# Performance work log

Measured on AMD Instinct MI355X. Metric: run time of the kernel, lower is better.

The kernel has to match this reference:

```python
import math
import jax, jax.numpy as jnp
import numpy as np

B, N, CS, CZ, CH, H, PQ, PV = 1, 4096, 512, 128, 64, 16, 4, 8
BQ, BK = 32, 128
NB = N // BQ
CZ4 = CZ // 4
INF = 100000.0
EPS = 1e-8


def quat_to_rot(q):
    w, x, y, z = q[..., 0], q[..., 1], q[..., 2], q[..., 3]
    return jnp.stack([
        jnp.stack([1 - 2 * (y * y + z * z), 2 * (x * y - w * z), 2 * (x * z + w * y)], -1),
        jnp.stack([2 * (x * y + w * z), 1 - 2 * (x * x + z * z), 2 * (y * z - w * x)], -1),
        jnp.stack([2 * (x * z - w * y), 2 * (y * z + w * x), 1 - 2 * (x * x + y * y)], -1),
    ], -2)


def setup_inputs() -> dict:
    key = jax.random.key(0)
    ks = jax.random.split(key, 16)
    s = jax.random.normal(ks[0], (B, N, CS), jnp.float32)
    z = jax.random.normal(ks[1], (B, NB, BQ, BK, CZ), jnp.float32)
    trans = jax.random.normal(ks[2], (B, N, 3), jnp.float32) * 10.0
    quat = jax.random.normal(ks[3], (B, N, 4), jnp.float32)
    quat = quat / jnp.linalg.norm(quat, axis=-1, keepdims=True)
    rots = quat_to_rot(quat)
    s_mask = jnp.ones((B, N), jnp.float32)
    pad = (BK - BQ) // 2  # key window centered on each query block
    key_idx = (jnp.arange(NB)[:, None] * BQ - pad + jnp.arange(BK)[None, :]).astype(jnp.int32)

    def w(k, shp):
        return jax.random.normal(k, shp, jnp.float32) * (1.0 / math.sqrt(shp[0]))

    return {
        's': s, 'z': z, 'trans': trans, 'rots': rots, 's_mask': s_mask, 'key_idx': key_idx,
        'Wq': w(ks[4], (CS, H * CH)), 'Wk': w(ks[5], (CS, H * CH)), 'Wv': w(ks[6], (CS, H * CH)),
        'Wqp': w(ks[7], (CS, H * PQ * 3)), 'Wkvp': w(ks[8], (CS, H * (PQ + PV) * 3)),
        'Wb': w(ks[9], (CZ, H)), 'Wdz': w(ks[10], (CZ, CZ4)),
        'head_weights': jnp.full((H,), float(np.log(np.e - 1.0)), jnp.float32),  # softplus^-1(1)
        'Wout': w(ks[11], (H * (CZ4 + CH + PV * 4), CS)),
        'g_s': jnp.ones((CS,), jnp.float32), 'b_s': jnp.zeros((CS,), jnp.float32),
        'g_z': jnp.ones((CZ,), jnp.float32), 'b_z': jnp.zeros((CZ,), jnp.float32),
    }


def _ln(x, g, b):
    m = jnp.mean(x, -1, keepdims=True)
    v = jnp.mean((x - m) ** 2, -1, keepdims=True)
    return (x - m) * jax.lax.rsqrt(v + 1e-5) * g + b


def _ipa(s, z, trans, rots, s_mask, key_idx, Wq, Wk, Wv, Wqp, Wkvp, Wb, Wdz,
         head_weights, Wout, g_s, b_s, g_z, b_z):
    s_n = _ln(s, g_s, b_s)
    z_n = _ln(z, g_z, b_z)

    valid = (key_idx >= 0) & (key_idx < N)            # [NB, BK]
    idx = jnp.clip(key_idx, 0, N - 1)
    vf = valid.astype(s.dtype)[None]                  # [1, NB, BK]

    def gk(x):  # gather key window: [B,N,...] -> [B,NB,BK,...]
        return x[:, idx]

    sq = s_n.reshape(B, NB, BQ, CS)
    sk = gk(s_n) * vf[..., None]                      # zero-pad out-of-range keys

    tq = trans.reshape(B, NB, BQ, 3)
    rq = rots.reshape(B, NB, BQ, 3, 3)
    tk = gk(trans) * vf[..., None]
    rk = jnp.where(valid[None, :, :, None, None], gk(rots), jnp.eye(3, dtype=rots.dtype))

    q = (sq @ Wq).reshape(B, NB, BQ, H, CH)
    k = (sk @ Wk).reshape(B, NB, BK, H, CH)
    v = (sk @ Wv).reshape(B, NB, BK, H, CH)

    q_pts = (sq @ Wqp).reshape(B, NB, BQ, H * PQ, 3)
    q_pts = jnp.einsum('bnqij,bnqpj->bnqpi', rq, q_pts) + tq[:, :, :, None, :]
    q_pts = q_pts.reshape(B, NB, BQ, H, PQ, 3)

    kv_pts = (sk @ Wkvp).reshape(B, NB, BK, H * (PQ + PV), 3)
    kv_pts = jnp.einsum('bnkij,bnkpj->bnkpi', rk, kv_pts) + tk[:, :, :, None, :]
    kv_pts = kv_pts.reshape(B, NB, BK, H, PQ + PV, 3)
    k_pts, v_pts = kv_pts[..., :PQ, :], kv_pts[..., PQ:, :]

    bias = jnp.einsum('bnqkc,ch->bnqkh', z_n, Wb)
    a = jnp.einsum('bnqhc,bnkhc->bnqkh', q, k) * math.sqrt(1.0 / (3 * CH))
    a = a + math.sqrt(1.0 / 3) * bias

    disp = q_pts[:, :, :, None] - k_pts[:, :, None]   # [B,NB,BQ,BK,H,PQ,3]
    pt_att = jnp.sum(disp ** 2, -1)                   # [B,NB,BQ,BK,H,PQ]
    hw = jax.nn.softplus(head_weights) * math.sqrt(1.0 / (3 * (PQ * 9.0 / 2)))
    pt_att = -0.5 * jnp.sum(pt_att * hw[:, None], -1)  # [B,NB,BQ,BK,H]

    qm = s_mask.reshape(B, NB, BQ)
    km = gk(s_mask) * vf
    amask = INF * (qm[:, :, :, None] * km[:, :, None, :] - 1.0)

    a = a + pt_att + amask[..., None]
    a = jax.nn.softmax(jnp.swapaxes(a, -1, -2), axis=-1)  # [B,NB,BQ,H,BK]

    o = jnp.einsum('bnqhk,bnkhc->bnqhc', a, v).reshape(B, NB, BQ, H * CH)

    o_pt = jnp.einsum('bnqhk,bnkhpc->bnqhpc', a, v_pts)
    o_pt = jnp.einsum('bnqji,bnqhpj->bnqhpi', rq, o_pt - tq[:, :, :, None, None, :])
    o_pt_norm = jnp.sqrt(jnp.sum(o_pt ** 2, -1) + EPS).reshape(B, NB, BQ, H * PV)
    o_pt = o_pt.reshape(B, NB, BQ, H * PV * 3)

    pair_z = z_n @ Wdz                                # [B,NB,BQ,BK,CZ4]
    o_pair = jnp.einsum('bnqhk,bnqkc->bnqhc', a, pair_z).reshape(B, NB, BQ, H * CZ4)

    out = jnp.concatenate([o, o_pt, o_pt_norm, o_pair], -1) @ Wout
    return out.reshape(B, N, CS)


def reference(s, z, trans, rots, s_mask, key_idx, Wq, Wk, Wv, Wqp, Wkvp, Wb, Wdz,
              head_weights, Wout, g_s, b_s, g_z, b_z):
    return _ipa(s, z, trans, rots, s_mask, key_idx, Wq, Wk, Wv, Wqp, Wkvp, Wb, Wdz,
                head_weights, Wout, g_s, b_s, g_z, b_z)
```

## Files before the change

### kernel.cpp

```cpp
#include <hip/hip_runtime.h>
#include <math.h>

#define D_N 4096
#define PBW 3072
#define PPW 768
#define OFFK 1024
#define OFFV 2048
#define CATW 2048

typedef __bf16 bf16_t;
typedef __bf16 bf16x8 __attribute__((ext_vector_type(8)));
typedef __bf16 bf16x4 __attribute__((ext_vector_type(4)));
typedef float f32x4 __attribute__((ext_vector_type(4)));

__device__ __forceinline__ void gld16(const void* g, void* l) {
    __builtin_amdgcn_global_load_lds((const __attribute__((address_space(1))) unsigned int*)g,
                                     (__attribute__((address_space(3))) unsigned int*)l, 16, 0, 0);
}

__global__ __launch_bounds__(256) void k_wcatT(const float* __restrict__ Wq, const float* __restrict__ Wk,
    const float* __restrict__ Wv, const float* __restrict__ Wqp, const float* __restrict__ Wkvp,
    bf16_t* __restrict__ out)
{
    __shared__ float T[64][65];
    int c0 = blockIdx.x * 64;
    int r0 = blockIdx.y * 64;
    const float* src; int ld, coff;
    if (c0 < 1024)      { src = Wq;   ld = 1024; coff = c0; }
    else if (c0 < 2048) { src = Wk;   ld = 1024; coff = c0 - 1024; }
    else if (c0 < 3072) { src = Wv;   ld = 1024; coff = c0 - 2048; }
    else if (c0 < 3264) { src = Wqp;  ld = 192;  coff = c0 - 3072; }
    else                { src = Wkvp; ld = 576;  coff = c0 - 3264; }
    int tid = threadIdx.x;
    {
        int rr = tid >> 2, cb = (tid & 3) * 16;
        const float* p = src + (size_t)(r0 + rr) * ld + coff + cb;
        #pragma unroll
        for (int i = 0; i < 4; ++i)
            *(float4*)&T[rr][cb + i * 4] = *(const float4*)(p + i * 4);
    }
    __syncthreads();
    {
        int cc = tid >> 2, rb = (tid & 3) * 16;
        bf16_t* o = out + (size_t)(c0 + cc) * 512 + r0 + rb;
        bf16x8 o0, o1;
        #pragma unroll
        for (int j = 0; j < 8; ++j) o0[j] = (bf16_t)T[rb + j][cc];
        #pragma unroll
        for (int j = 0; j < 8; ++j) o1[j] = (bf16_t)T[rb + 8 + j][cc];
        *(bf16x8*)(o) = o0;
        *(bf16x8*)(o + 8) = o1;
    }
}

__global__ __launch_bounds__(256) void t_cvt(const float* __restrict__ in, bf16_t* __restrict__ out,
    int R, int C)
{
    __shared__ float T[64][65];
    int r0 = blockIdx.y * 64, c0 = blockIdx.x * 64;
    int tid = threadIdx.x;
    {
        int rr = tid >> 2;
        int cb = (tid & 3) * 16;
        const float* p = in + (size_t)(r0 + rr) * C + c0 + cb;
        #pragma unroll
        for (int i = 0; i < 4; ++i) {
            float4 v = *(const float4*)(p + i * 4);
            *(float4*)&T[rr][cb + i * 4] = v;
        }
    }
    __syncthreads();
    {
        int cc = tid >> 2;
        int rb = (tid & 3) * 16;
        bf16_t* o = out + (size_t)(c0 + cc) * R + r0 + rb;
        bf16x8 o0, o1;
        #pragma unroll
        for (int j = 0; j < 8; ++j) o0[j] = (bf16_t)T[rb + j][cc];
        #pragma unroll
        for (int j = 0; j < 8; ++j) o1[j] = (bf16_t)T[rb + 8 + j][cc];
        *(bf16x8*)(o) = o0;
        *(bf16x8*)(o + 8) = o1;
    }
}

__global__ __launch_bounds__(256) void k_wz2(const float* __restrict__ Wb, const float* __restrict__ Wdz,
    const float* __restrict__ gz, const float* __restrict__ bz,
    bf16_t* __restrict__ WzT, float* __restrict__ Kv)
{
    int i = blockIdx.x * 256 + threadIdx.x;
    if (i < 6144) {
        int j = i >> 7, c = i & 127;
        float w = (j < 16) ? Wb[c * 16 + j] : Wdz[c * 32 + (j - 16)];
        WzT[i] = (bf16_t)(gz[c] * w);
    }
    if (blockIdx.x == 0 && threadIdx.x < 48) {
        int j = threadIdx.x;
        float acc = 0.f;
        for (int c = 0; c < 128; ++c) {
            float w = (j < 16) ? Wb[c * 16 + j] : Wdz[c * 32 + (j - 16)];
            acc += bz[c] * w;
        }
        Kv[j] = acc;
    }
}

__global__ __launch_bounds__(64) void k_ln_s(const float* __restrict__ s, const float* __restrict__ g,
    const float* __restrict__ b, bf16_t* __restrict__ out)
{
    int row = blockIdx.x;
    int lane = threadIdx.x;
    const float4* p = (const float4*)(s + (size_t)row * 512);
    float4 v0 = p[lane];
    float4 v1 = p[lane + 64];
    float sum = v0.x + v0.y + v0.z + v0.w + v1.x + v1.y + v1.z + v1.w;
    float sq  = v0.x*v0.x + v0.y*v0.y + v0.z*v0.z + v0.w*v0.w
              + v1.x*v1.x + v1.y*v1.y + v1.z*v1.z + v1.w*v1.w;
    #pragma unroll
    for (int off = 1; off < 64; off <<= 1) {
        sum += __shfl_xor(sum, off);
        sq  += __shfl_xor(sq, off);
    }
    float m = sum * (1.0f / 512.0f);
    float var = sq * (1.0f / 512.0f) - m * m;
    float rs = rsqrtf(var + 1e-5f);
    int c = lane * 4;
    int c2 = 256 + lane * 4;
    bf16x4 r0, r1;
    r0[0] = (bf16_t)((v0.x - m) * rs * g[c+0] + b[c+0]);
    r0[1] = (bf16_t)((v0.y - m) * rs * g[c+1] + b[c+1]);
    r0[2] = (bf16_t)((v0.z - m) * rs * g[c+2] + b[c+2]);
    r0[3] = (bf16_t)((v0.w - m) * rs * g[c+3] + b[c+3]);
    r1[0] = (bf16_t)((v1.x - m) * rs * g[c2+0] + b[c2+0]);
    r1[1] = (bf16_t)((v1.y - m) * rs * g[c2+1] + b[c2+1]);
    r1[2] = (bf16_t)((v1.z - m) * rs * g[c2+2] + b[c2+2]);
    r1[3] = (bf16_t)((v1.w - m) * rs * g[c2+3] + b[c2+3]);
    *(bf16x4*)(out + (size_t)row * 512 + c)  = r0;
    *(bf16x4*)(out + (size_t)row * 512 + c2) = r1;
}

__global__ __launch_bounds__(256) void gemm_proj(const bf16_t* __restrict__ A, const bf16_t* __restrict__ BT,
    bf16_t* __restrict__ projb, float* __restrict__ projp, int K)
{
    __shared__ bf16_t As[128][40];
    __shared__ bf16_t Bs[128][40];
    const int tid = threadIdx.x, lane = tid & 63, w = tid >> 6;
    const int row0 = blockIdx.y * 128, col0 = blockIdx.x * 128;
    const int wr = (w >> 1) * 64, wc = (w & 1) * 64;
    const int srow = tid >> 1, skoff = (tid & 1) * 16;
    const bf16_t* Ap = A + (size_t)(row0 + srow) * K + skoff;
    const bf16_t* Bp = BT + (size_t)(col0 + srow) * K + skoff;
    f32x4 acc[4][4];
    #pragma unroll
    for (int m = 0; m < 4; ++m)
        #pragma unroll
        for (int n = 0; n < 4; ++n) acc[m][n] = (f32x4){0.f,0.f,0.f,0.f};
    for (int k0 = 0; k0 < K; k0 += 32) {
        uint4 a0 = *(const uint4*)(Ap + k0);
        uint4 a1 = *(const uint4*)(Ap + k0 + 8);
        uint4 b0 = *(const uint4*)(Bp + k0);
        uint4 b1 = *(const uint4*)(Bp + k0 + 8);
        __syncthreads();
        *(uint4*)&As[srow][skoff]     = a0;
        *(uint4*)&As[srow][skoff + 8] = a1;
        *(uint4*)&Bs[srow][skoff]     = b0;
        *(uint4*)&Bs[srow][skoff + 8] = b1;
        __syncthreads();
        bf16x8 af[4], bfr[4];
        #pragma unroll
        for (int m = 0; m < 4; ++m) af[m]  = *(const bf16x8*)&As[wr + m*16 + (lane & 15)][(lane >> 4) * 8];
        #pragma unroll
        for (int n = 0; n < 4; ++n) bfr[n] = *(const bf16x8*)&Bs[wc + n*16 + (lane & 15)][(lane >> 4) * 8];
        #pragma unroll
        for (int m = 0; m < 4; ++m)
            #pragma unroll
            for (int n = 0; n < 4; ++n)
                acc[m][n] = __builtin_amdgcn_mfma_f32_16x16x32_bf16(af[m], bfr[n], acc[m][n], 0, 0, 0);
    }
    if (col0 < 3072) {
        #pragma unroll
        for (int m = 0; m < 4; ++m)
            #pragma unroll
            for (int n = 0; n < 4; ++n)
                #pragma unroll
                for (int i = 0; i < 4; ++i)
                    projb[(size_t)(row0 + wr + m*16 + (lane >> 4)*4 + i) * PBW + col0 + wc + n*16 + (lane & 15)]
                        = (bf16_t)acc[m][n][i];
    } else {
        #pragma unroll
        for (int m = 0; m < 4; ++m)
            #pragma unroll
            for (int n = 0; n < 4; ++n)
                #pragma unroll
                for (int i = 0; i < 4; ++i)
                    projp[(size_t)(row0 + wr + m*16 + (lane >> 4)*4 + i) * PPW + col0 - 3072 + wc + n*16 + (lane & 15)]
                        = acc[m][n][i];
    }
}

__global__ __launch_bounds__(256) void gemm_bf64(const bf16_t* __restrict__ A, const bf16_t* __restrict__ BT,
    float* __restrict__ C, int M, int N, int K)
{
    __shared__ bf16_t As[128][40];
    __shared__ bf16_t Bs[64][40];
    const int tid = threadIdx.x, lane = tid & 63, w = tid >> 6;
    const int row0 = blockIdx.y * 128, col0 = blockIdx.x * 64;
    const int wr = w * 32;
    const int srow = tid >> 1, skoff = (tid & 1) * 16;
    const int brow = tid >> 2, bkoff = (tid & 3) * 8;
    const bf16_t* Ap = A + (size_t)(row0 + srow) * K + skoff;
    const bf16_t* Bp = BT + (size_t)(col0 + brow) * K + bkoff;
    f32x4 acc[2][4];
    #pragma unroll
    for (int m = 0; m < 2; ++m)
        #pragma unroll
        for (int n = 0; n < 4; ++n) acc[m][n] = (f32x4){0.f,0.f,0.f,0.f};
    for (int k0 = 0; k0 < K; k0 += 32) {
        uint4 a0 = *(const uint4*)(Ap + k0);
        uint4 a1 = *(const uint4*)(Ap + k0 + 8);
        uint4 b0 = *(const uint4*)(Bp + k0);
        __syncthreads();
        *(uint4*)&As[srow][skoff]     = a0;
        *(uint4*)&As[srow][skoff + 8] = a1;
        *(uint4*)&Bs[brow][bkoff]     = b0;
        __syncthreads();
        bf16x8 af[2], bfr[4];
        #pragma unroll
        for (int m = 0; m < 2; ++m) af[m]  = *(const bf16x8*)&As[wr + m*16 + (lane & 15)][(lane >> 4) * 8];
        #pragma unroll
        for (int n = 0; n < 4; ++n) bfr[n] = *(const bf16x8*)&Bs[n*16 + (lane & 15)][(lane >> 4) * 8];
        #pragma unroll
        for (int m = 0; m < 2; ++m)
            #pragma unroll
            for (int n = 0; n < 4; ++n)
                acc[m][n] = __builtin_amdgcn_mfma_f32_16x16x32_bf16(af[m], bfr[n], acc[m][n], 0, 0, 0);
    }
    #pragma unroll
    for (int m = 0; m < 2; ++m)
        #pragma unroll
        for (int n = 0; n < 4; ++n)
            #pragma unroll
            for (int i = 0; i < 4; ++i)
                C[(size_t)(row0 + wr + m*16 + (lane >> 4)*4 + i) * N + col0 + n*16 + (lane & 15)] = acc[m][n][i];
}

__global__ __launch_bounds__(256) void k_rot(float* __restrict__ projp, const float* __restrict__ rots,
    const float* __restrict__ trans)
{
    int row = blockIdx.x;
    int tid = threadIdx.x;
    const float* R = rots + (size_t)row * 9;
    const float* t = trans + (size_t)row * 3;
    float* base = projp + (size_t)row * PPW + tid * 3;
    float x = base[0], y = base[1], z = base[2];
    base[0] = R[0] * x + R[1] * y + R[2] * z + t[0];
    base[1] = R[3] * x + R[4] * y + R[5] * z + t[1];
    base[2] = R[6] * x + R[7] * y + R[8] * z + t[2];
}

__global__ __launch_bounds__(256) void k_zbias3(const float* __restrict__ z,
    const bf16_t* __restrict__ WzT, const float* __restrict__ Kv,
    float* __restrict__ biasT, bf16_t* __restrict__ pzT)
{
    __shared__ __align__(16) float zbuf[2][64][128];
    const int tid = threadIdx.x, lane = tid & 63, w = tid >> 6;
    const int r16 = lane & 15, kg = lane >> 4;
    bf16x8 bfz[3][4];
    #pragma unroll
    for (int nt = 0; nt < 3; ++nt)
        #pragma unroll
        for (int kc = 0; kc < 4; ++kc)
            bfz[nt][kc] = *(const bf16x8*)(WzT + (size_t)(nt * 16 + r16) * 128 + kc * 32 + kg * 8);
    float K0 = Kv[r16], K1 = Kv[16 + r16], K2 = Kv[32 + r16];
    asm volatile("s_waitcnt vmcnt(0)" ::: "memory");

    const int gid = blockIdx.x * 4 + w;
    const char* zb = (const char*)z + (size_t)gid * 64 * 512;
    char* lb0 = (char*)&zbuf[0][w * 16][0];
    char* lb1 = (char*)&zbuf[1][w * 16][0];

#define STAGE(i, lb) { \
    const char* gp_ = zb + (size_t)(i) * 8192 + lane * 16; \
    _Pragma("unroll") \
    for (int c_ = 0; c_ < 8; ++c_) gld16(gp_ + c_ * 1024, (lb) + c_ * 1024); }

#define PROCESS(i, b) { \
    const float* rp = &zbuf[b][w * 16 + r16][kg * 8]; \
    float4 za[4], zc[4]; \
    float sum = 0.f, sq = 0.f; \
    _Pragma("unroll") \
    for (int kc = 0; kc < 4; ++kc) { \
        float4 a_ = *(const float4*)(rp + kc * 32); \
        float4 b_ = *(const float4*)(rp + kc * 32 + 4); \
        za[kc] = a_; zc[kc] = b_; \
        sum += a_.x + a_.y + a_.z + a_.w + b_.x + b_.y + b_.z + b_.w; \
        sq  += a_.x*a_.x + a_.y*a_.y + a_.z*a_.z + a_.w*a_.w + b_.x*b_.x + b_.y*b_.y + b_.z*b_.z + b_.w*b_.w; \
    } \
    sum += __shfl_xor(sum, 16); sq += __shfl_xor(sq, 16); \
    sum += __shfl_xor(sum, 32); sq += __shfl_xor(sq, 32); \
    float m_ = sum * (1.0f / 128.0f); \
    float rs_ = rsqrtf(sq * (1.0f / 128.0f) - m_ * m_ + 1e-5f); \
    bf16x8 af[4]; \
    _Pragma("unroll") \
    for (int kc = 0; kc < 4; ++kc) { \
        af[kc][0] = (bf16_t)((za[kc].x - m_) * rs_); \
        af[kc][1] = (bf16_t)((za[kc].y - m_) * rs_); \
        af[kc][2] = (bf16_t)((za[kc].z - m_) * rs_); \
        af[kc][3] = (bf16_t)((za[kc].w - m_) * rs_); \
        af[kc][4] = (bf16_t)((zc[kc].x - m_) * rs_); \
        af[kc][5] = (bf16_t)((zc[kc].y - m_) * rs_); \
        af[kc][6] = (bf16_t)((zc[kc].z - m_) * rs_); \
        af[kc][7] = (bf16_t)((zc[kc].w - m_) * rs_); \
    } \
    f32x4 acc0 = (f32x4){0.f,0.f,0.f,0.f}; \
    f32x4 acc1 = (f32x4){0.f,0.f,0.f,0.f}; \
    f32x4 acc2 = (f32x4){0.f,0.f,0.f,0.f}; \
    _Pragma("unroll") \
    for (int kc = 0; kc < 4; ++kc) { \
        acc0 = __builtin_amdgcn_mfma_f32_16x16x32_bf16(af[kc], bfz[0][kc], acc0, 0, 0, 0); \
        acc1 = __builtin_amdgcn_mfma_f32_16x16x32_bf16(af[kc], bfz[1][kc], acc1, 0, 0, 0); \
        acc2 = __builtin_amdgcn_mfma_f32_16x16x32_bf16(af[kc], bfz[2][kc], acc2, 0, 0, 0); \
    } \
    const int t_ = gid * 4 + (i); \
    const int rowq_ = t_ >> 3; \
    const int k0_ = ((t_ & 7) << 4) + kg * 4; \
    float4 bw = {acc0[0] + K0, acc0[1] + K0, acc0[2] + K0, acc0[3] + K0}; \
    *(float4*)&biasT[((size_t)rowq_ * 16 + r16) * 128 + k0_] = bw; \
    bf16x4 p1, p2; \
    _Pragma("unroll") \
    for (int i2 = 0; i2 < 4; ++i2) { p1[i2] = (bf16_t)(acc1[i2] + K1); p2[i2] = (bf16_t)(acc2[i2] + K2); } \
    *(bf16x4*)&pzT[((size_t)rowq_ * 32 + r16) * 128 + k0_] = p1; \
    *(bf16x4*)&pzT[((size_t)rowq_ * 32 + 16 + r16) * 128 + k0_] = p2; }

    STAGE(0, lb0);
    STAGE(1, lb1);
    asm volatile("s_waitcnt vmcnt(8)" ::: "memory");
    PROCESS(0, 0);
    STAGE(2, lb0);
    asm volatile("s_waitcnt vmcnt(11)" ::: "memory");
    PROCESS(1, 1);
    STAGE(3, lb1);
    asm volatile("s_waitcnt vmcnt(11)" ::: "memory");
    PROCESS(2, 0);
    asm volatile("s_waitcnt vmcnt(3)" ::: "memory");
    PROCESS(3, 1);
#undef STAGE
#undef PROCESS
}

__global__ __launch_bounds__(256) void k_attn3(
    const bf16_t* __restrict__ projb, const float* __restrict__ projp,
    const float* __restrict__ biasT, const float* __restrict__ rots,
    const float* __restrict__ trans, const float* __restrict__ smask,
    const int* __restrict__ kidx, const float* __restrict__ hwraw,
    bf16_t* __restrict__ catb, bf16_t* __restrict__ Pbf)
{
    __shared__ __align__(16) char uni[26112];
    __shared__ float att[32][132];
    __shared__ float kp_s[128][12];
    __shared__ float qp_s[32][12];
    __shared__ bf16_t Ps[32][136];
    __shared__ float optmp[32][33];
    __shared__ float km_s[128];
    __shared__ float qm_s[32];
    __shared__ int   rows_s[128];

    bf16_t (*Qs)[72]  = (bf16_t(*)[72])uni;
    bf16_t (*Ks)[72]  = (bf16_t(*)[72])(uni + 32 * 72 * 2);
    bf16_t (*Vt)[136] = (bf16_t(*)[136])uni;

    const int nblk = blockIdx.x;
    const int h = blockIdx.y;
    const int tid = threadIdx.x;
    const int lane = tid & 63;
    const int w = tid >> 6;
    const int rowq0 = nblk * 32;
    const float hw = log1pf(__expf(hwraw[h])) * 0.13608276348795434f;

    if (tid < 128) {
        int ki = kidx[nblk * 128 + tid];
        int valid = (ki >= 0 && ki < D_N);
        int rr = ki < 0 ? 0 : (ki > D_N - 1 ? D_N - 1 : ki);
        rows_s[tid] = rr;
        km_s[tid] = valid ? smask[rr] : 0.0f;
    } else if (tid < 160) {
        qm_s[tid - 128] = smask[rowq0 + tid - 128];
    }
    __syncthreads();
    {
        int q = tid >> 3, cg = (tid & 7) * 8;
        *(bf16x8*)&Qs[q][cg] = *(const bf16x8*)(projb + (size_t)(rowq0 + q) * PBW + h * 64 + cg);
    }
    if (tid < 128) {
        int q = tid >> 2, dg = (tid & 3) * 3;
        const float* p = projp + (size_t)(rowq0 + q) * PPW + h * 12 + dg;
        qp_s[q][dg + 0] = p[0]; qp_s[q][dg + 1] = p[1]; qp_s[q][dg + 2] = p[2];
    }
    {
        int krow = tid >> 1, cg = (tid & 1) * 32;
        const bf16_t* p = projb + (size_t)rows_s[krow] * PBW + OFFK + h * 64 + cg;
        #pragma unroll
        for (int u = 0; u < 4; ++u)
            *(bf16x8*)&Ks[krow][cg + u * 8] = *(const bf16x8*)(p + u * 8);
        const float* pk = projp + (size_t)rows_s[krow] * PPW + 192 + h * 36 + (tid & 1) * 6;
        int dg = (tid & 1) * 6;
        #pragma unroll
        for (int u = 0; u < 6; ++u) kp_s[krow][dg + u] = pk[u];
    }
    __syncthreads();
    {
        #pragma unroll
        for (int j = 0; j < 4; ++j) {
            int T = w * 4 + j;
            int m = T & 1, n = T >> 1;
            f32x4 acc = (f32x4){0.f,0.f,0.f,0.f};
            #pragma unroll
            for (int kc = 0; kc < 2; ++kc) {
                bf16x8 a = *(const bf16x8*)&Qs[m*16 + (lane & 15)][kc*32 + (lane >> 4) * 8];
                bf16x8 b = *(const bf16x8*)&Ks[n*16 + (lane & 15)][kc*32 + (lane >> 4) * 8];
                acc = __builtin_amdgcn_mfma_f32_16x16x32_bf16(a, b, acc, 0, 0, 0);
            }
            #pragma unroll
            for (int i = 0; i < 4; ++i)
                att[m*16 + (lane >> 4)*4 + i][n*16 + (lane & 15)] = acc[i];
        }
    }
    __syncthreads();
    {
        int krow = tid >> 1, cg = (tid & 1) * 32;
        const bf16_t* p = projb + (size_t)rows_s[krow] * PBW + OFFV + h * 64 + cg;
        #pragma unroll
        for (int u4 = 0; u4 < 4; ++u4) {
            bf16x8 v = *(const bf16x8*)(p + u4 * 8);
            #pragma unroll
            for (int j = 0; j < 8; ++j) Vt[cg + u4 * 8 + j][krow] = v[j];
        }
        const float* pv = projp + (size_t)rows_s[krow] * PPW + 192 + h * 36 + 12 + (tid & 1) * 12;
        #pragma unroll
        for (int u = 0; u < 3; ++u) {
            float4 v = *(const float4*)(pv + u * 4);
            int rb = 64 + (tid & 1) * 12 + u * 4;
            Vt[rb + 0][krow] = (bf16_t)v.x;
            Vt[rb + 1][krow] = (bf16_t)v.y;
            Vt[rb + 2][krow] = (bf16_t)v.z;
            Vt[rb + 3][krow] = (bf16_t)v.w;
        }
        {
            int r = 88 + (tid >> 5), c = (tid & 31) * 4;
            bf16x4 zz; zz[0]=(bf16_t)0.f; zz[1]=(bf16_t)0.f; zz[2]=(bf16_t)0.f; zz[3]=(bf16_t)0.f;
            *(bf16x4*)&Vt[r][c] = zz;
        }
        int q = tid >> 3, kg = tid & 7;
        float qp[12];
        #pragma unroll
        for (int e = 0; e < 12; ++e) qp[e] = qp_s[q][e];
        float qm = qm_s[q];
        const float* bT = biasT + ((size_t)(rowq0 + q) * 16 + h) * 128;
        #pragma unroll
        for (int j2 = 0; j2 < 16; ++j2) {
            int k = kg + j2 * 8;
            float4 k0 = *(const float4*)&kp_s[k][0];
            float4 k1 = *(const float4*)&kp_s[k][4];
            float4 k2 = *(const float4*)&kp_s[k][8];
            float d0 = qp[0]-k0.x, d1 = qp[1]-k0.y, d2_ = qp[2]-k0.z, d3 = qp[3]-k0.w;
            float d4 = qp[4]-k1.x, d5 = qp[5]-k1.y, d6 = qp[6]-k1.z, d7 = qp[7]-k1.w;
            float d8 = qp[8]-k2.x, d9 = qp[9]-k2.y, d10 = qp[10]-k2.z, d11 = qp[11]-k2.w;
            float dd = d0*d0+d1*d1+d2_*d2_+d3*d3+d4*d4+d5*d5+d6*d6+d7*d7+d8*d8+d9*d9+d10*d10+d11*d11;
            float val = att[q][k] * 0.07216878364870323f
                      + 0.5773502691896258f * bT[k]
                      + 100000.0f * (qm * km_s[k] - 1.0f)
                      - 0.5f * hw * dd;
            att[q][k] = val;
        }
    }
    __syncthreads();
    {
        int q = tid >> 3, kg = tid & 7;
        float l[16];
        #pragma unroll
        for (int j2 = 0; j2 < 16; ++j2) l[j2] = att[q][kg + j2 * 8];
        float mx = l[0];
        #pragma unroll
        for (int j2 = 1; j2 < 16; ++j2) mx = fmaxf(mx, l[j2]);
        mx = fmaxf(mx, __shfl_xor(mx, 1));
        mx = fmaxf(mx, __shfl_xor(mx, 2));
        mx = fmaxf(mx, __shfl_xor(mx, 4));
        float se = 0.f;
        #pragma unroll
        for (int j2 = 0; j2 < 16; ++j2) { l[j2] = __expf(l[j2] - mx); se += l[j2]; }
        se += __shfl_xor(se, 1);
        se += __shfl_xor(se, 2);
        se += __shfl_xor(se, 4);
        float inv = 1.0f / se;
        bf16_t* pg = Pbf + ((size_t)(rowq0 + q) * 16 + h) * 128;
        #pragma unroll
        for (int j2 = 0; j2 < 16; ++j2) {
            bf16_t pb = (bf16_t)(l[j2] * inv);
            Ps[q][kg + j2 * 8] = pb;
            pg[kg + j2 * 8] = pb;
        }
    }
    __syncthreads();
    {
        #pragma unroll
        for (int j = 0; j < 3; ++j) {
            int T = w * 3 + j;
            int m = T & 1, n = T >> 1;
            f32x4 acc = (f32x4){0.f,0.f,0.f,0.f};
            #pragma unroll
            for (int kc = 0; kc < 4; ++kc) {
                bf16x8 a = *(const bf16x8*)&Ps[m*16 + (lane & 15)][kc*32 + (lane >> 4) * 8];
                bf16x8 b = *(const bf16x8*)&Vt[n*16 + (lane & 15)][kc*32 + (lane >> 4) * 8];
                acc = __builtin_amdgcn_mfma_f32_16x16x32_bf16(a, b, acc, 0, 0, 0);
            }
            int rowb = m * 16 + (lane >> 4) * 4;
            int col = lane & 15;
            if (n < 4) {
                #pragma unroll
                for (int i = 0; i < 4; ++i)
                    catb[(size_t)(rowq0 + rowb + i) * CATW + h * 64 + n * 16 + col] = (bf16_t)acc[i];
            } else {
                #pragma unroll
                for (int i = 0; i < 4; ++i)
                    optmp[rowb + i][(n - 4) * 16 + col] = acc[i];
            }
        }
    }
    __syncthreads();
    {
        int q = tid >> 3, pp = tid & 7;
        float sx = optmp[q][pp * 3 + 0];
        float sy = optmp[q][pp * 3 + 1];
        float sz = optmp[q][pp * 3 + 2];
        const float* R = rots + (size_t)(rowq0 + q) * 9;
        const float* t = trans + (size_t)(rowq0 + q) * 3;
        float x = sx - t[0], y = sy - t[1], z2 = sz - t[2];
        float ox = R[0] * x + R[3] * y + R[6] * z2;
        float oy = R[1] * x + R[4] * y + R[7] * z2;
        float oz = R[2] * x + R[5] * y + R[8] * z2;
        bf16_t* cp = catb + (size_t)(rowq0 + q) * CATW;
        cp[1024 + h * 24 + pp * 3 + 0] = (bf16_t)ox;
        cp[1024 + h * 24 + pp * 3 + 1] = (bf16_t)oy;
        cp[1024 + h * 24 + pp * 3 + 2] = (bf16_t)oz;
        cp[1408 + h * 8 + pp] = (bf16_t)sqrtf(ox * ox + oy * oy + oz * oz + 1e-8f);
    }
}

__global__ __launch_bounds__(256) void k_opair(const bf16_t* __restrict__ Pbf,
    const bf16_t* __restrict__ pzT, bf16_t* __restrict__ catb)
{
    int tid = threadIdx.x, lane = tid & 63, w = tid >> 6;
    size_t rowq = (size_t)blockIdx.x * 4 + w;
    const bf16_t* Pp = Pbf + rowq * 2048;
    const bf16_t* zp = pzT + rowq * 4096;
    bf16x8 pa[4];
    #pragma unroll
    for (int kc = 0; kc < 4; ++kc)
        pa[kc] = *(const bf16x8*)(Pp + (size_t)(lane & 15) * 128 + kc * 32 + (lane >> 4) * 8);
    #pragma unroll
    for (int ct = 0; ct < 2; ++ct) {
        f32x4 acc = (f32x4){0.f,0.f,0.f,0.f};
        #pragma unroll
        for (int kc = 0; kc < 4; ++kc) {
            bf16x8 b = *(const bf16x8*)(zp + (size_t)(ct * 16 + (lane & 15)) * 128 + kc * 32 + (lane >> 4) * 8);
            acc = __builtin_amdgcn_mfma_f32_16x16x32_bf16(pa[kc], b, acc, 0, 0, 0);
        }
        #pragma unroll
        for (int i = 0; i < 4; ++i) {
            int hh = (lane >> 4) * 4 + i;
            catb[rowq * CATW + 1536 + hh * 32 + ct * 16 + (lane & 15)] = (bf16_t)acc[i];
        }
    }
}

extern "C" void kernel_launch(void* const* d_in, const int* in_sizes, int n_in,
                              void* d_out, int out_size, void* d_ws, size_t ws_size,
                              hipStream_t stream)
{
    (void)in_sizes; (void)n_in; (void)out_size;
    const float* s     = (const float*)d_in[0];
    const float* z     = (const float*)d_in[1];
    const float* trans = (const float*)d_in[2];
    const float* rots  = (const float*)d_in[3];
    const float* smask = (const float*)d_in[4];
    const int*   kidx  = (const int*)d_in[5];
    const float* Wq    = (const float*)d_in[6];
    const float* Wk    = (const float*)d_in[7];
    const float* Wv    = (const float*)d_in[8];
    const float* Wqp   = (const float*)d_in[9];
    const float* Wkvp  = (const float*)d_in[10];
    const float* Wb    = (const float*)d_in[11];
    const float* Wdz   = (const float*)d_in[12];
    const float* hw    = (const float*)d_in[13];
    const float* Wout  = (const float*)d_in[14];
    const float* g_s   = (const float*)d_in[15];
    const float* b_s   = (const float*)d_in[16];
    const float* g_z   = (const float*)d_in[17];
    const float* b_z   = (const float*)d_in[18];

    char* ws = (char*)d_ws;
    bf16_t* projb = (bf16_t*)(ws);
    float*  projp = (float*)(ws + 25165824);
    float*  biasT = (float*)(ws + 37748736);
    bf16_t* wcatT = (bf16_t*)(ws + 71303168);
    bf16_t* s_nb  = (bf16_t*)(ws + 75235328);
    bf16_t* pzT   = (bf16_t*)(ws + 79429632);
    bf16_t* Pbf   = (bf16_t*)(ws + 112984064);
    bf16_t* catb  = (bf16_t*)(ws + 129761280);
    bf16_t* WoutT = (bf16_t*)(ws + 146538496);
    bf16_t* WzT   = (bf16_t*)(ws + 148635648);
    float*  Kv    = (float*)(ws + 148647936);
    if (ws_size < (size_t)148648128) return;
    float* out = (float*)d_out;

    k_wcatT<<<dim3(60, 8), 256, 0, stream>>>(Wq, Wk, Wv, Wqp, Wkvp, wcatT);
    t_cvt<<<dim3(8, 32), 256, 0, stream>>>(Wout, WoutT, 2048, 512);
    k_wz2<<<24, 256, 0, stream>>>(Wb, Wdz, g_z, b_z, WzT, Kv);
    k_ln_s<<<4096, 64, 0, stream>>>(s, g_s, b_s, s_nb);
    gemm_proj<<<dim3(30, 32), 256, 0, stream>>>(s_nb, wcatT, projb, projp, 512);
    k_rot<<<4096, 256, 0, stream>>>(projp, rots, trans);
    k_zbias3<<<2048, 256, 0, stream>>>(z, WzT, Kv, biasT, pzT);
    k_attn3<<<dim3(128, 16), 256, 0, stream>>>(projb, projp, biasT, rots, trans, smask, kidx, hw, catb, Pbf);
    k_opair<<<1024, 256, 0, stream>>>(Pbf, pzT, catb);
    gemm_bf64<<<dim3(8, 32), 256, 0, stream>>>(catb, WoutT, out, 4096, 512, 2048);
}
```

Measured before the change: 237.3 us.

## Merge prep kernels, fuse rotation into z-bias kernel, use LDS-direct GEMM loads

Folds the four weight/LN prep kernels into one launch and moves the point rotation into extra blocks of the z-bias kernel, cutting launch count. Both GEMMs now load tiles with global_load_lds into unpadded LDS, and the output GEMM moves to 128x128 tiles with a 4x4 MFMA layout per wave. The attention grid is flattened and swizzled so consecutive workgroups take different heads. Risks include LDS bank conflicts from the unpadded tiles, only 128 blocks for the output GEMM, and the rotation blocks possibly running concurrently with z-bias blocks in a way that changes timing.

```diff
diff --git a/kernel.cpp b/kernel.cpp
--- a/kernel.cpp
+++ b/kernel.cpp
@@ -18,159 +18,133 @@
                                      (__attribute__((address_space(3))) unsigned int*)l, 16, 0, 0);
 }
 
-__global__ __launch_bounds__(256) void k_wcatT(const float* __restrict__ Wq, const float* __restrict__ Wk,
-    const float* __restrict__ Wv, const float* __restrict__ Wqp, const float* __restrict__ Wkvp,
-    bf16_t* __restrict__ out)
+__global__ __launch_bounds__(256) void k_prep(
+    const float* __restrict__ Wq, const float* __restrict__ Wk, const float* __restrict__ Wv,
+    const float* __restrict__ Wqp, const float* __restrict__ Wkvp, const float* __restrict__ Wout,
+    const float* __restrict__ Wb, const float* __restrict__ Wdz,
+    const float* __restrict__ gz, const float* __restrict__ bz,
+    const float* __restrict__ s, const float* __restrict__ g_s, const float* __restrict__ b_s,
+    bf16_t* __restrict__ wcatT, bf16_t* __restrict__ WoutT,
+    bf16_t* __restrict__ WzT, float* __restrict__ Kv, bf16_t* __restrict__ s_nb)
 {
     __shared__ float T[64][65];
-    int c0 = blockIdx.x * 64;
-    int r0 = blockIdx.y * 64;
-    const float* src; int ld, coff;
-    if (c0 < 1024)      { src = Wq;   ld = 1024; coff = c0; }
-    else if (c0 < 2048) { src = Wk;   ld = 1024; coff = c0 - 1024; }
-    else if (c0 < 3072) { src = Wv;   ld = 1024; coff = c0 - 2048; }
-    else if (c0 < 3264) { src = Wqp;  ld = 192;  coff = c0 - 3072; }
-    else                { src = Wkvp; ld = 576;  coff = c0 - 3264; }
-    int tid = threadIdx.x;
-    {
-        int rr = tid >> 2, cb = (tid & 3) * 16;
-        const float* p = src + (size_t)(r0 + rr) * ld + coff + cb;
-        #pragma unroll
-        for (int i = 0; i < 4; ++i)
-            *(float4*)&T[rr][cb + i * 4] = *(const float4*)(p + i * 4);
-    }
-    __syncthreads();
-    {
-        int cc = tid >> 2, rb = (tid & 3) * 16;
-        bf16_t* o = out + (size_t)(c0 + cc) * 512 + r0 + rb;
-        bf16x8 o0, o1;
-        #pragma unroll
-        for (int j = 0; j < 8; ++j) o0[j] = (bf16_t)T[rb + j][cc];
-        #pragma unroll
-        for (int j = 0; j < 8; ++j) o1[j] = (bf16_t)T[rb + 8 + j][cc];
-        *(bf16x8*)(o) = o0;
-        *(bf16x8*)(o + 8) = o1;
-    }
-}
-
-__global__ __launch_bounds__(256) void t_cvt(const float* __restrict__ in, bf16_t* __restrict__ out,
-    int R, int C)
+    const int bx = blockIdx.x;
+    const int tid = threadIdx.x;
+    if (bx < 736) {
+        const float* src; int ld, coff, r0;
+        bf16_t* dst; int Rdst;
+        if (bx < 480) {
+            int c0 = (bx % 60) * 64;
+            r0 = (bx / 60) * 64;
+            if (c0 < 1024)      { src = Wq;   ld = 1024; coff = c0; }
+            else if (c0 < 2048) { src = Wk;   ld = 1024; coff = c0 - 1024; }
+            else if (c0 < 3072) { src = Wv;   ld = 1024; coff = c0 - 2048; }
+            else if (c0 < 3264) { src = Wqp;  ld = 192;  coff = c0 - 3072; }
+            else                { src = Wkvp; ld = 576;  coff = c0 - 3264; }
+            dst = wcatT + (size_t)c0 * 512; Rdst = 512;
+        } else {
+            int b = bx - 480;
+            int c0 = (b & 7) * 64;
+            r0 = (b >> 3) * 64;
+            src = Wout; ld = 512; coff = c0;
+            dst = WoutT + (size_t)c0 * 2048; Rdst = 2048;
+        }
+        {
+            int rr = tid >> 2, cb = (tid & 3) * 16;
+            const float* p = src + (size_t)(r0 + rr) * ld + coff + cb;
+            #pragma unroll
+            for (int i = 0; i < 4; ++i)
+                *(float4*)&T[rr][cb + i * 4] = *(const float4*)(p + i * 4);
+        }
+        __syncthreads();
+        {
+            int cc = tid >> 2, rb = (tid & 3) * 16;
+            bf16_t* o = dst + (size_t)cc * Rdst + r0 + rb;
+            bf16x8 o0, o1;
+            #pragma unroll
+            for (int j = 0; j < 8; ++j) o0[j] = (bf16_t)T[rb + j][cc];
+            #pragma unroll
+            for (int j = 0; j < 8; ++j) o1[j] = (bf16_t)T[rb + 8 + j][cc];
+            *(bf16x8*)(o) = o0;
+            *(bf16x8*)(o + 8) = o1;
+        }
+    } else if (bx == 736) {
+        for (int i = tid; i < 6144; i += 256) {
+            int j = i >> 7, c = i & 127;
+            float w = (j < 16) ? Wb[c * 16 + j] : Wdz[c * 32 + (j - 16)];
+            WzT[i] = (bf16_t)(gz[c] * w);
+        }
+        if (tid < 48) {
+            int j = tid;
+            float acc = 0.f;
+            for (int c = 0; c < 128; ++c) {
+                float w = (j < 16) ? Wb[c * 16 + j] : Wdz[c * 32 + (j - 16)];
+                acc += bz[c] * w;
+            }
+            Kv[j] = acc;
+        }
+    } else {
+        int row = (bx - 737) * 4 + (tid >> 6);
+        int lane = tid & 63;
+        const float4* p = (const float4*)(s + (size_t)row * 512);
+        float4 v0 = p[lane];
+        float4 v1 = p[lane + 64];
+        float sum = v0.x + v0.y + v0.z + v0.w + v1.x + v1.y + v1.z + v1.w;
+        float sq  = v0.x*v0.x + v0.y*v0.y + v0.z*v0.z + v0.w*v0.w
+                  + v1.x*v1.x + v1.y*v1.y + v1.z*v1.z + v1.w*v1.w;
+        #pragma unroll
+        for (int off = 1; off < 64; off <<= 1) {
+            sum += __shfl_xor(sum, off);
+            sq  += __shfl_xor(sq, off);
+        }
+        float m = sum * (1.0f / 512.0f);
+        float var = sq * (1.0f / 512.0f) - m * m;
+        float rs = rsqrtf(var + 1e-5f);
+        int c = lane * 4;
+        int c2 = 256 + lane * 4;
+        bf16x4 r0, r1;
+        r0[0] = (bf16_t)((v0.x - m) * rs * g_s[c+0] + b_s[c+0]);
+        r0[1] = (bf16_t)((v0.y - m) * rs * g_s[c+1] + b_s[c+1]);
+        r0[2] = (bf16_t)((v0.z - m) * rs * g_s[c+2] + b_s[c+2]);
+        r0[3] = (bf16_t)((v0.w - m) * rs * g_s[c+3] + b_s[c+3]);
+        r1[0] = (bf16_t)((v1.x - m) * rs * g_s[c2+0] + b_s[c2+0]);
+        r1[1] = (bf16_t)((v1.y - m) * rs * g_s[c2+1] + b_s[c2+1]);
+        r1[2] = (bf16_t)((v1.z - m) * rs * g_s[c2+2] + b_s[c2+2]);
+        r1[3] = (bf16_t)((v1.w - m) * rs * g_s[c2+3] + b_s[c2+3]);
+        *(bf16x4*)(s_nb + (size_t)row * 512 + c)  = r0;
+        *(bf16x4*)(s_nb + (size_t)row * 512 + c2) = r1;
+    }
+}
+
+__global__ __launch_bounds__(256) void gemm_proj(const bf16_t* __restrict__ A, const bf16_t* __restrict__ BT,
+    bf16_t* __restrict__ projb, float* __restrict__ projp)
 {
-    __shared__ float T[64][65];
-    int r0 = blockIdx.y * 64, c0 = blockIdx.x * 64;
-    int tid = threadIdx.x;
-    {
-        int rr = tid >> 2;
-        int cb = (tid & 3) * 16;
-        const float* p = in + (size_t)(r0 + rr) * C + c0 + cb;
-        #pragma unroll
-        for (int i = 0; i < 4; ++i) {
-            float4 v = *(const float4*)(p + i * 4);
-            *(float4*)&T[rr][cb + i * 4] = v;
-        }
-    }
-    __syncthreads();
-    {
-        int cc = tid >> 2;
-        int rb = (tid & 3) * 16;
-        bf16_t* o = out + (size_t)(c0 + cc) * R + r0 + rb;
-        bf16x8 o0, o1;
-        #pragma unroll
-        for (int j = 0; j < 8; ++j) o0[j] = (bf16_t)T[rb + j][cc];
-        #pragma unroll
-        for (int j = 0; j < 8; ++j) o1[j] = (bf16_t)T[rb + 8 + j][cc];
-        *(bf16x8*)(o) = o0;
-        *(bf16x8*)(o + 8) = o1;
-    }
-}
-
-__global__ __launch_bounds__(256) void k_wz2(const float* __restrict__ Wb, const float* __restrict__ Wdz,
-    const float* __restrict__ gz, const float* __restrict__ bz,
-    bf16_t* __restrict__ WzT, float* __restrict__ Kv)
-{
-    int i = blockIdx.x * 256 + threadIdx.x;
-    if (i < 6144) {
-        int j = i >> 7, c = i & 127;
-        float w = (j < 16) ? Wb[c * 16 + j] : Wdz[c * 32 + (j - 16)];
-        WzT[i] = (bf16_t)(gz[c] * w);
-    }
-    if (blockIdx.x == 0 && threadIdx.x < 48) {
-        int j = threadIdx.x;
-        float acc = 0.f;
-        for (int c = 0; c < 128; ++c) {
-            float w = (j < 16) ? Wb[c * 16 + j] : Wdz[c * 32 + (j - 16)];
-            acc += bz[c] * w;
-        }
-        Kv[j] = acc;
-    }
-}
-
-__global__ __launch_bounds__(64) void k_ln_s(const float* __restrict__ s, const float* __restrict__ g,
-    const float* __restrict__ b, bf16_t* __restrict__ out)
-{
-    int row = blockIdx.x;
-    int lane = threadIdx.x;
-    const float4* p = (const float4*)(s + (size_t)row * 512);
-    float4 v0 = p[lane];
-    float4 v1 = p[lane + 64];
-    float sum = v0.x + v0.y + v0.z + v0.w + v1.x + v1.y + v1.z + v1.w;
-    float sq  = v0.x*v0.x + v0.y*v0.y + v0.z*v0.z + v0.w*v0.w
-              + v1.x*v1.x + v1.y*v1.y + v1.z*v1.z + v1.w*v1.w;
-    #pragma unroll
-    for (int off = 1; off < 64; off <<= 1) {
-        sum += __shfl_xor(sum, off);
-        sq  += __shfl_xor(sq, off);
-    }
-    float m = sum * (1.0f / 512.0f);
-    float var = sq * (1.0f / 512.0f) - m * m;
-    float rs = rsqrtf(var + 1e-5f);
-    int c = lane * 4;
-    int c2 = 256 + lane * 4;
-    bf16x4 r0, r1;
-    r0[0] = (bf16_t)((v0.x - m) * rs * g[c+0] + b[c+0]);
-    r0[1] = (bf16_t)((v0.y - m) * rs * g[c+1] + b[c+1]);
-    r0[2] = (bf16_t)((v0.z - m) * rs * g[c+2] + b[c+2]);
-    r0[3] = (bf16_t)((v0.w - m) * rs * g[c+3] + b[c+3]);
-    r1[0] = (bf16_t)((v1.x - m) * rs * g[c2+0] + b[c2+0]);
-    r1[1] = (bf16_t)((v1.y - m) * rs * g[c2+1] + b[c2+1]);
-    r1[2] = (bf16_t)((v1.z - m) * rs * g[c2+2] + b[c2+2]);
-    r1[3] = (bf16_t)((v1.w - m) * rs * g[c2+3] + b[c2+3]);
-    *(bf16x4*)(out + (size_t)row * 512 + c)  = r0;
-    *(bf16x4*)(out + (size_t)row * 512 + c2) = r1;
-}
-
-__global__ __launch_bounds__(256) void gemm_proj(const bf16_t* __restrict__ A, const bf16_t* __restrict__ BT,
-    bf16_t* __restrict__ projb, float* __restrict__ projp, int K)
-{
-    __shared__ bf16_t As[128][40];
-    __shared__ bf16_t Bs[128][40];
+    __shared__ bf16_t Asl[128][32];
+    __shared__ bf16_t Bsl[128][32];
     const int tid = threadIdx.x, lane = tid & 63, w = tid >> 6;
     const int row0 = blockIdx.y * 128, col0 = blockIdx.x * 128;
     const int wr = (w >> 1) * 64, wc = (w & 1) * 64;
-    const int srow = tid >> 1, skoff = (tid & 1) * 16;
-    const bf16_t* Ap = A + (size_t)(row0 + srow) * K + skoff;
-    const bf16_t* Bp = BT + (size_t)(col0 + srow) * K + skoff;
+    const int K = 512;
+    const int sr = lane >> 2, k8 = (lane & 3) * 8;
+    const bf16_t* Ab = A + (size_t)(row0 + w * 32 + sr) * K + k8;
+    const bf16_t* Bb = BT + (size_t)(col0 + w * 32 + sr) * K + k8;
     f32x4 acc[4][4];
     #pragma unroll
     for (int m = 0; m < 4; ++m)
         #pragma unroll
         for (int n = 0; n < 4; ++n) acc[m][n] = (f32x4){0.f,0.f,0.f,0.f};
     for (int k0 = 0; k0 < K; k0 += 32) {
-        uint4 a0 = *(const uint4*)(Ap + k0);
-        uint4 a1 = *(const uint4*)(Ap + k0 + 8);
-        uint4 b0 = *(const uint4*)(Bp + k0);
-        uint4 b1 = *(const uint4*)(Bp + k0 + 8);
         __syncthreads();
-        *(uint4*)&As[srow][skoff]     = a0;
-        *(uint4*)&As[srow][skoff + 8] = a1;
-        *(uint4*)&Bs[srow][skoff]     = b0;
-        *(uint4*)&Bs[srow][skoff + 8] = b1;
+        gld16(Ab + k0,          &Asl[w * 32][0]);
+        gld16(Ab + k0 + 16 * K, &Asl[w * 32 + 16][0]);
+        gld16(Bb + k0,          &Bsl[w * 32][0]);
+        gld16(Bb + k0 + 16 * K, &Bsl[w * 32 + 16][0]);
         __syncthreads();
         bf16x8 af[4], bfr[4];
         #pragma unroll
-        for (int m = 0; m < 4; ++m) af[m]  = *(const bf16x8*)&As[wr + m*16 + (lane & 15)][(lane >> 4) * 8];
-        #pragma unroll
-        for (int n = 0; n < 4; ++n) bfr[n] = *(const bf16x8*)&Bs[wc + n*16 + (lane & 15)][(lane >> 4) * 8];
+        for (int m = 0; m < 4; ++m) af[m]  = *(const bf16x8*)&Asl[wr + m*16 + (lane & 15)][(lane >> 4) * 8];
+        #pragma unroll
+        for (int n = 0; n < 4; ++n) bfr[n] = *(const bf16x8*)&Bsl[wc + n*16 + (lane & 15)][(lane >> 4) * 8];
         #pragma unroll
         for (int m = 0; m < 4; ++m)
             #pragma unroll
@@ -198,72 +172,77 @@
     }
 }
 
-__global__ __launch_bounds__(256) void gemm_bf64(const bf16_t* __restrict__ A, const bf16_t* __restrict__ BT,
-    float* __restrict__ C, int M, int N, int K)
+__global__ __launch_bounds__(256) void gemm_out(const bf16_t* __restrict__ A, const bf16_t* __restrict__ BT,
+    float* __restrict__ C)
 {
-    __shared__ bf16_t As[128][40];
-    __shared__ bf16_t Bs[64][40];
+    __shared__ bf16_t Asl[128][32];
+    __shared__ bf16_t Bsl[128][32];
     const int tid = threadIdx.x, lane = tid & 63, w = tid >> 6;
-    const int row0 = blockIdx.y * 128, col0 = blockIdx.x * 64;
-    const int wr = w * 32;
-    const int srow = tid >> 1, skoff = (tid & 1) * 16;
-    const int brow = tid >> 2, bkoff = (tid & 3) * 8;
-    const bf16_t* Ap = A + (size_t)(row0 + srow) * K + skoff;
-    const bf16_t* Bp = BT + (size_t)(col0 + brow) * K + bkoff;
-    f32x4 acc[2][4];
+    const int row0 = blockIdx.y * 128, col0 = blockIdx.x * 128;
+    const int wr = (w >> 1) * 64, wc = (w & 1) * 64;
+    const int K = 2048;
+    const int sr = lane >> 2, k8 = (lane & 3) * 8;
+    const bf16_t* Ab = A + (size_t)(row0 + w * 32 + sr) * K + k8;
+    const bf16_t* Bb = BT + (size_t)(col0 + w * 32 + sr) * K + k8;
+    f32x4 acc[4][4];
     #pragma unroll
-    for (int m = 0; m < 2; ++m)
+    for (int m = 0; m < 4; ++m)
         #pragma unroll
         for (int n = 0; n < 4; ++n) acc[m][n] = (f32x4){0.f,0.f,0.f,0.f};
     for (int k0 = 0; k0 < K; k0 += 32) {
-        uint4 a0 = *(const uint4*)(Ap + k0);
-        uint4 a1 = *(const uint4*)(Ap + k0 + 8);
-        uint4 b0 = *(const uint4*)(Bp + k0);
         __syncthreads();
-        *(uint4*)&As[srow][skoff]     = a0;
-        *(uint4*)&As[srow][skoff + 8] = a1;
-        *(uint4*)&Bs[brow][bkoff]     = b0;
+        gld16(Ab + k0,          &Asl[w * 32][0]);
+        gld16(Ab + k0 + 16 * K, &Asl[w * 32 + 16][0]);
+        gld16(Bb + k0,          &Bsl[w * 32][0]);
+        gld16(Bb + k0 + 16 * K, &Bsl[w * 32 + 16][0]);
         __syncthreads();
-        bf16x8 af[2], bfr[4];
-        #pragma unroll
-        for (int m = 0; m < 2; ++m) af[m]  = *(const bf16x8*)&As[wr + m*16 + (lane & 15)][(lane >> 4) * 8];
-        #pragma unroll
-        for (int n = 0; n < 4; ++n) bfr[n] = *(const bf16x8*)&Bs[n*16 + (lane & 15)][(lane >> 4) * 8];
-        #pragma unroll
-        for (int m = 0; m < 2; ++m)
+        bf16x8 af[4], bfr[4];
+        #pragma unroll
+        for (int m = 0; m < 4; ++m) af[m]  = *(const bf16x8*)&Asl[wr + m*16 + (lane & 15)][(lane >> 4) * 8];
+        #pragma unroll
+        for (int n = 0; n < 4; ++n) bfr[n] = *(const bf16x8*)&Bsl[wc + n*16 + (lane & 15)][(lane >> 4) * 8];
+        #pragma unroll
+        for (int m = 0; m < 4; ++m)
             #pragma unroll
             for (int n = 0; n < 4; ++n)
                 acc[m][n] = __builtin_amdgcn_mfma_f32_16x16x32_bf16(af[m], bfr[n], acc[m][n], 0, 0, 0);
     }
     #pragma unroll
-    for (int m = 0; m < 2; ++m)
+    for (int m = 0; m < 4; ++m)
         #pragma unroll
         for (int n = 0; n < 4; ++n)
             #pragma unroll
             for (int i = 0; i < 4; ++i)
-                C[(size_t)(row0 + wr + m*16 + (lane >> 4)*4 + i) * N + col0 + n*16 + (lane & 15)] = acc[m][n][i];
-}
-
-__global__ __launch_bounds__(256) void k_rot(float* __restrict__ projp, const float* __restrict__ rots,
-    const float* __restrict__ trans)
-{
-    int row = blockIdx.x;
-    int tid = threadIdx.x;
-    const float* R = rots + (size_t)row * 9;
-    const float* t = trans + (size_t)row * 3;
-    float* base = projp + (size_t)row * PPW + tid * 3;
-    float x = base[0], y = base[1], z = base[2];
-    base[0] = R[0] * x + R[1] * y + R[2] * z + t[0];
-    base[1] = R[3] * x + R[4] * y + R[5] * z + t[1];
-    base[2] = R[6] * x + R[7] * y + R[8] * z + t[2];
-}
-
-__global__ __launch_bounds__(256) void k_zbias3(const float* __restrict__ z,
+                C[(size_t)(row0 + wr + m*16 + (lane >> 4)*4 + i) * 512 + col0 + wc + n*16 + (lane & 15)] = acc[m][n][i];
+}
+
+__global__ __launch_bounds__(256) void k_zrot(const float* __restrict__ z,
     const bf16_t* __restrict__ WzT, const float* __restrict__ Kv,
-    float* __restrict__ biasT, bf16_t* __restrict__ pzT)
+    float* __restrict__ biasT, bf16_t* __restrict__ pzT,
+    float* __restrict__ projp, const float* __restrict__ rots, const float* __restrict__ trans)
 {
     __shared__ __align__(16) float zbuf[2][64][128];
     const int tid = threadIdx.x, lane = tid & 63, w = tid >> 6;
+    if (blockIdx.x >= 2048) {
+        int row = (blockIdx.x - 2048) * 4 + (tid >> 6);
+        const float* R = rots + (size_t)row * 9;
+        const float* t = trans + (size_t)row * 3;
+        float R0=R[0],R1=R[1],R2=R[2],R3=R[3],R4=R[4],R5=R[5],R6=R[6],R7=R[7],R8=R[8];
+        float t0=t[0],t1=t[1],t2=t[2];
+        float* base = projp + (size_t)row * PPW + lane * 12;
+        float4 a = *(const float4*)(base);
+        float4 b = *(const float4*)(base + 4);
+        float4 c = *(const float4*)(base + 8);
+        float x0=a.x,y0=a.y,z0=a.z, x1=a.w,y1=b.x,z1=b.y, x2=b.z,y2=b.w,z2=c.x, x3=c.y,y3=c.z,z3=c.w;
+        a.x = R0*x0+R1*y0+R2*z0+t0; a.y = R3*x0+R4*y0+R5*z0+t1; a.z = R6*x0+R7*y0+R8*z0+t2;
+        a.w = R0*x1+R1*y1+R2*z1+t0; b.x = R3*x1+R4*y1+R5*z1+t1; b.y = R6*x1+R7*y1+R8*z1+t2;
+        b.z = R0*x2+R1*y2+R2*z2+t0; b.w = R3*x2+R4*y2+R5*z2+t1; c.x = R6*x2+R7*y2+R8*z2+t2;
+        c.y = R0*x3+R1*y3+R2*z3+t0; c.z = R3*x3+R4*y3+R5*z3+t1; c.w = R6*x3+R7*y3+R8*z3+t2;
+        *(float4*)(base) = a;
+        *(float4*)(base + 4) = b;
+        *(float4*)(base + 8) = c;
+        return;
+    }
     const int r16 = lane & 15, kg = lane >> 4;
     bf16x8 bfz[3][4];
     #pragma unroll
@@ -369,8 +348,10 @@
     bf16_t (*Ks)[72]  = (bf16_t(*)[72])(uni + 32 * 72 * 2);
     bf16_t (*Vt)[136] = (bf16_t(*)[136])uni;
 
-    const int nblk = blockIdx.x;
-    const int h = blockIdx.y;
+    const int wgid = blockIdx.x;
+    const int swz = (wgid & 7) * 256 + (wgid >> 3);
+    const int h = swz >> 7;
+    const int nblk = swz & 127;
     const int tid = threadIdx.x;
     const int lane = tid & 63;
     const int w = tid >> 6;
@@ -613,14 +594,11 @@
     if (ws_size < (size_t)148648128) return;
     float* out = (float*)d_out;
 
-    k_wcatT<<<dim3(60, 8), 256, 0, stream>>>(Wq, Wk, Wv, Wqp, Wkvp, wcatT);
-    t_cvt<<<dim3(8, 32), 256, 0, stream>>>(Wout, WoutT, 2048, 512);
-    k_wz2<<<24, 256, 0, stream>>>(Wb, Wdz, g_z, b_z, WzT, Kv);
-    k_ln_s<<<4096, 64, 0, stream>>>(s, g_s, b_s, s_nb);
-    gemm_proj<<<dim3(30, 32), 256, 0, stream>>>(s_nb, wcatT, projb, projp, 512);
-    k_rot<<<4096, 256, 0, stream>>>(projp, rots, trans);
-    k_zbias3<<<2048, 256, 0, stream>>>(z, WzT, Kv, biasT, pzT);
-    k_attn3<<<dim3(128, 16), 256, 0, stream>>>(projb, projp, biasT, rots, trans, smask, kidx, hw, catb, Pbf);
+    k_prep<<<1761, 256, 0, stream>>>(Wq, Wk, Wv, Wqp, Wkvp, Wout, Wb, Wdz, g_z, b_z,
+                                     s, g_s, b_s, wcatT, WoutT, WzT, Kv, s_nb);
+    gemm_proj<<<dim3(30, 32), 256, 0, stream>>>(s_nb, wcatT, projb, projp);
+    k_zrot<<<3072, 256, 0, stream>>>(z, WzT, Kv, biasT, pzT, projp, rots, trans);
+    k_attn3<<<2048, 256, 0, stream>>>(projb, projp, biasT, rots, trans, smask, kidx, hw, catb, Pbf);
     k_opair<<<1024, 256, 0, stream>>>(Pbf, pzT, catb);
-    gemm_bf64<<<dim3(8, 32), 256, 0, stream>>>(catb, WoutT, out, 4096, 512, 2048);
-}
+    gemm_out<<<dim3(4, 32), 256, 0, stream>>>(catb, WoutT, out);
+}
```

Result: faster. 230.8 us (-2.8%).
